# Performance work log

Measured on AMD Instinct MI355X. Metric: run time of the kernel, lower is better.

The kernel has to match this reference:

```python
import jax, jax.numpy as jnp
import numpy as np

B, T, D, H = 64, 512, 768, 96


def setup_inputs() -> dict:
    key = jax.random.key(0)
    kx, kq, kk, kv = jax.random.split(key, 4)
    x = jax.random.normal(kx, (B, T, D), dtype=jnp.float32)
    # Linear weights stored as [in, out]; scaled like torch default init
    s = 1.0 / np.sqrt(D)
    Wq = jax.random.normal(kq, (D, H), dtype=jnp.float32) * s
    Wk = jax.random.normal(kk, (D, H), dtype=jnp.float32) * s
    Wv = jax.random.normal(kv, (D, H), dtype=jnp.float32) * s
    return {"x": x, "Wq": Wq, "Wk": Wk, "Wv": Wv}


def reference(x, Wq, Wk, Wv):
    # q,k,v: [B,T,H]
    q = jnp.einsum('btd,dh->bth', x, Wq)
    k = jnp.einsum('btd,dh->bth', x, Wk)
    v = jnp.einsum('btd,dh->bth', x, Wv)
    scale = 1.0 / jnp.sqrt(jnp.array(q.shape[-1], dtype=x.dtype))
    # scores: [B,T,T]
    wei = jnp.einsum('bqh,bkh->bqk', q, k) * scale
    causal = jnp.tril(jnp.ones((T, T), dtype=bool))
    wei = jnp.where(causal, wei, jnp.array(-jnp.inf, dtype=wei.dtype))
    attn = jax.nn.softmax(wei, axis=-1)
    return jnp.einsum('bqk,bkh->bqh', attn, v)
```

## Files before the change

### kernel.cpp

```cpp
#include <hip/hip_runtime.h>
#include <hip/hip_bf16.h>
#include <math.h>

#define B_ 64
#define T_ 512
#define D_ 768
#define H_ 96
#define M_ (B_*T_)

typedef __attribute__((ext_vector_type(8))) short short8;
typedef __attribute__((ext_vector_type(4))) float f32x4;
typedef __attribute__((ext_vector_type(4))) unsigned uint4v;

__device__ __forceinline__ short f2bf(float f) {
  unsigned u = __float_as_uint(f);
  unsigned r = (u + 0x7FFFu + ((u >> 16) & 1u)) >> 16;
  return (short)r;
}

__device__ __forceinline__ unsigned cvtpk(float lo, float hi) {
  unsigned r;
  asm("v_cvt_pk_bf16_f32 %0, %1, %2" : "=v"(r) : "v"(lo), "v"(hi));
  return r;
}

__device__ __forceinline__ void gl16(const void* g, void* l) {
  __builtin_amdgcn_global_load_lds(
      (const __attribute__((address_space(1))) unsigned*)g,
      (__attribute__((address_space(3))) unsigned*)l, 16, 0, 0);
}

__global__ __launch_bounds__(256) void wt_kernel(
    const float* __restrict__ Wq, const float* __restrict__ Wk,
    const float* __restrict__ Wv, short* __restrict__ wt)
{
  int id = blockIdx.x * 256 + threadIdx.x;
  if (id >= 3*H_*D_) return;
  int n = id % 288;
  int k = id / 288;
  int mi = n / 96, cc = n % 96;
  const float* Wm = (mi == 0) ? Wq : ((mi == 1) ? Wk : Wv);
  wt[(size_t)n * D_ + k] = f2bf(Wm[(size_t)k * H_ + cc]);
}

#define BKP 32
#define ABYTES 8192
#define BBYTES 9216

__global__ __launch_bounds__(256) void qkv_mfma_kernel(
    const float* __restrict__ x, const short* __restrict__ wt,
    short* __restrict__ qb, short* __restrict__ kb, short* __restrict__ vb)
{
  __shared__ float As[2][64][32];
  __shared__ short Bs[2][144][32];

  const int t    = threadIdx.x;
  const int row0 = blockIdx.x * 64;
  const int cg   = blockIdx.y;
  const int lane = t & 63;
  const int w    = t >> 6;
  const int l15  = lane & 15;
  const int l4   = lane >> 4;

  auto stageA = [&](int buf, int k0) {
    #pragma unroll
    for (int i = 0; i < 2; ++i) {
      int inst = w * 2 + i;
      int row  = inst * 8 + (lane >> 3);
      int c16  = (lane & 7) ^ ((lane >> 3) & 7);
      const char* g = (const char*)(x + (size_t)(row0 + row) * D_ + k0) + c16 * 16;
      char* l = (char*)&As[buf][0][0] + inst * 1024 + lane * 16;
      gl16(g, l);
    }
  };
  auto stageB = [&](int buf, int k0) {
    #pragma unroll
    for (int i = 0; i < 3; ++i) {
      int inst = w + 4 * i;
      if (inst < 9) {
        int row = inst * 16 + (lane >> 2);
        int c16 = (lane & 3) ^ ((lane >> 2) & 3);
        const char* g = (const char*)(wt + (size_t)(cg * 144 + row) * D_ + k0) + c16 * 16;
        char* l = (char*)&Bs[buf][0][0] + inst * 1024 + lane * 16;
        gl16(g, l);
      }
    }
  };

  f32x4 acc[9];
  #pragma unroll
  for (int ci = 0; ci < 9; ++ci) acc[ci] = (f32x4){0.f, 0.f, 0.f, 0.f};

  stageA(0, 0);
  stageB(0, 0);
  __syncthreads();

  const int arow = w * 16 + l15;
  const char* Abase = (const char*)&As[0][0][0];
  const char* Bbase = (const char*)&Bs[0][0][0];

  for (int ks = 0; ks < 24; ++ks) {
    int buf = ks & 1;
    if (ks + 1 < 24) { stageA(buf ^ 1, (ks + 1) * BKP); stageB(buf ^ 1, (ks + 1) * BKP); }

    const char* ab = Abase + (size_t)buf * ABYTES + arow * 128;
    float4 a0 = *reinterpret_cast<const float4*>(ab + (((l4 * 2 + 0) ^ (arow & 7)) * 16));
    float4 a1 = *reinterpret_cast<const float4*>(ab + (((l4 * 2 + 1) ^ (arow & 7)) * 16));
    uint4v uv;
    uv[0] = cvtpk(a0.x, a0.y); uv[1] = cvtpk(a0.z, a0.w);
    uv[2] = cvtpk(a1.x, a1.y); uv[3] = cvtpk(a1.z, a1.w);
    short8 af = *reinterpret_cast<short8*>(&uv);

    #pragma unroll
    for (int ci = 0; ci < 9; ++ci) {
      int brow = ci * 16 + l15;
      short8 bf = *reinterpret_cast<const short8*>(
          Bbase + (size_t)buf * BBYTES + brow * 64 + ((l4 ^ (brow & 3)) * 16));
      acc[ci] = __builtin_amdgcn_mfma_f32_16x16x32_bf16(af, bf, acc[ci], 0, 0, 0);
    }
    __syncthreads();
  }

  const int rbase = row0 + w * 16 + l4 * 4;
  #pragma unroll
  for (int ci = 0; ci < 9; ++ci) {
    int ncol = cg * 144 + ci * 16;
    int mi   = ncol / 96;
    int cc   = ncol % 96 + l15;
    short* Om = (mi == 0) ? qb : ((mi == 1) ? kb : vb);
    #pragma unroll
    for (int reg = 0; reg < 4; ++reg)
      Om[(size_t)(rbase + reg) * H_ + cc] = f2bf(acc[ci][reg]);
  }
}

#define QB 32
#define KVB 32
#define KSTR 104
#define VSTR 40
#define PSTR 40

__global__ __launch_bounds__(128) void attn_mfma_kernel(
    const short* __restrict__ qb, const short* __restrict__ kb,
    const short* __restrict__ vb, float* __restrict__ out)
{
  __shared__ short ks[KVB][KSTR];
  __shared__ short vs[H_][VSTR];
  __shared__ short ps[2][16][PSTR];

  const int t    = threadIdx.x;
  const int lane = t & 63;
  const int w    = t >> 6;
  const int l15  = lane & 15;
  const int l4   = lane >> 4;
  const int qi   = 15 - blockIdx.x;
  const int b    = blockIdx.y;
  const int q0   = qi * QB;

  short8 qf[3];
  {
    const short* qbase = qb + ((size_t)(b * T_) + q0 + w * 16 + l15) * H_;
    #pragma unroll
    for (int f = 0; f < 3; ++f)
      qf[f] = *reinterpret_cast<const short8*>(qbase + f * 32 + l4 * 8);
  }

  f32x4 acc[6];
  #pragma unroll
  for (int c = 0; c < 6; ++c) acc[c] = (f32x4){0.f, 0.f, 0.f, 0.f};
  float m_r[4] = {-INFINITY, -INFINITY, -INFINITY, -INFINITY};
  float l_r[4] = {0.f, 0.f, 0.f, 0.f};
  const float scale = 0.10206207261596576f;

  const int jmax = q0 + QB;
  for (int j0 = 0; j0 < jmax; j0 += KVB) {
    __syncthreads();
    {
      int row = t >> 2, seg = t & 3;
      const short* src = kb + ((size_t)(b * T_) + j0 + row) * H_ + seg * 24;
      short* dst = &ks[row][seg * 24];
      *reinterpret_cast<short8*>(dst)      = *reinterpret_cast<const short8*>(src);
      *reinterpret_cast<short8*>(dst + 8)  = *reinterpret_cast<const short8*>(src + 8);
      *reinterpret_cast<short8*>(dst + 16) = *reinterpret_cast<const short8*>(src + 16);
    }
    {
      #pragma unroll
      for (int i = 0; i < 3; ++i) {
        int c = t + i * 128;
        int tok = c / 12;
        int m   = c % 12;
        int h0  = m * 8;
        short8 v = *reinterpret_cast<const short8*>(
            vb + (size_t)(b * T_ + j0 + tok) * H_ + h0);
        int tokS = tok ^ ((m & 3) << 3);
        #pragma unroll
        for (int j = 0; j < 8; ++j) vs[h0 + j][tokS] = v[j];
      }
    }
    __syncthreads();

    f32x4 sfr[2];
    sfr[0] = (f32x4){0.f,0.f,0.f,0.f};
    sfr[1] = (f32x4){0.f,0.f,0.f,0.f};
    #pragma unroll
    for (int ct = 0; ct < 2; ++ct)
      #pragma unroll
      for (int f = 0; f < 3; ++f) {
        short8 kf = *reinterpret_cast<const short8*>(&ks[ct * 16 + l15][f * 32 + l4 * 8]);
        sfr[ct] = __builtin_amdgcn_mfma_f32_16x16x32_bf16(qf[f], kf, sfr[ct], 0, 0, 0);
      }

    const int qrow = q0 + w * 16 + l4 * 4;
    float p0[4], p1[4], fsc[4];
    #pragma unroll
    for (int reg = 0; reg < 4; ++reg) {
      float s0 = sfr[0][reg] * scale;
      float s1 = sfr[1][reg] * scale;
      if (j0 + l15      > qrow + reg) s0 = -INFINITY;
      if (j0 + l15 + 16 > qrow + reg) s1 = -INFINITY;
      float tm = fmaxf(s0, s1);
      #pragma unroll
      for (int o = 1; o < 16; o <<= 1) tm = fmaxf(tm, __shfl_xor(tm, o));
      float Mnew = fmaxf(m_r[reg], tm);
      p0[reg] = __expf(s0 - Mnew);
      p1[reg] = __expf(s1 - Mnew);
      float psum = p0[reg] + p1[reg];
      #pragma unroll
      for (int o = 1; o < 16; o <<= 1) psum += __shfl_xor(psum, o);
      fsc[reg] = __expf(m_r[reg] - Mnew);
      m_r[reg] = Mnew;
      l_r[reg] = l_r[reg] * fsc[reg] + psum;
    }
    #pragma unroll
    for (int c = 0; c < 6; ++c)
      #pragma unroll
      for (int reg = 0; reg < 4; ++reg) acc[c][reg] *= fsc[reg];

    #pragma unroll
    for (int reg = 0; reg < 4; ++reg) {
      ps[w][l4 * 4 + reg][l15]      = f2bf(p0[reg]);
      ps[w][l4 * 4 + reg][l15 + 16] = f2bf(p1[reg]);
    }
    short8 pa = *reinterpret_cast<const short8*>(&ps[w][l15][l4 * 8]);

    #pragma unroll
    for (int c = 0; c < 6; ++c) {
      int h = c * 16 + l15;
      short8 vf = *reinterpret_cast<const short8*>(
          &vs[h][(l4 ^ ((h >> 3) & 3)) * 8]);
      acc[c] = __builtin_amdgcn_mfma_f32_16x16x32_bf16(pa, vf, acc[c], 0, 0, 0);
    }
  }

  float inv[4];
  #pragma unroll
  for (int reg = 0; reg < 4; ++reg) inv[reg] = 1.f / l_r[reg];
  #pragma unroll
  for (int c = 0; c < 6; ++c) {
    #pragma unroll
    for (int reg = 0; reg < 4; ++reg) {
      size_t row = (size_t)(b * T_) + q0 + w * 16 + l4 * 4 + reg;
      out[row * H_ + c * 16 + l15] = acc[c][reg] * inv[reg];
    }
  }
}

extern "C" void kernel_launch(void* const* d_in, const int* in_sizes, int n_in,
                              void* d_out, int out_size, void* d_ws, size_t ws_size,
                              hipStream_t stream) {
  const float* x  = (const float*)d_in[0];
  const float* Wq = (const float*)d_in[1];
  const float* Wk = (const float*)d_in[2];
  const float* Wv = (const float*)d_in[3];

  short* wt = (short*)d_ws;
  short* qb = (short*)((char*)d_ws + 524288);
  short* kb = qb + (size_t)M_ * H_;
  short* vb = kb + (size_t)M_ * H_;
  float* outp = (float*)d_out;

  hipLaunchKernelGGL(wt_kernel, dim3((3*H_*D_ + 255)/256), dim3(256), 0, stream,
                     Wq, Wk, Wv, wt);
  hipLaunchKernelGGL(qkv_mfma_kernel, dim3(M_/64, 2), dim3(256), 0, stream,
                     x, wt, qb, kb, vb);
  hipLaunchKernelGGL(attn_mfma_kernel, dim3(T_/QB, B_), dim3(128), 0, stream,
                     qb, kb, vb, outp);
}
```

Measured before the change: 79.35 us.

## Load full bf16 x tile once per block and cover all 288 QKV columns

The QKV projection kernel now converts a whole 64x768 fp32 x tile to bf16 in shared memory at the start, and each block computes all 288 output columns instead of splitting them across two blocks. This halves global reads of x, which were previously duplicated across the two column groups, and removes the per-step fp32-to-bf16 conversion from the main loop. Each wave now computes a 32x144 tile (two row fragments), so every loaded B fragment feeds two MFMAs. The cost is about 96KB of LDS for A plus 36KB for B, which lowers occupancy. The A tile is also loaded synchronously up front with no overlap with compute.

```diff
diff --git a/kernel.cpp b/kernel.cpp
--- a/kernel.cpp
+++ b/kernel.cpp
@@ -44,93 +44,100 @@
 }
 
 #define BKP 32
-#define ABYTES 8192
-#define BBYTES 9216
+#define BBYTES 18432
 
 __global__ __launch_bounds__(256) void qkv_mfma_kernel(
     const float* __restrict__ x, const short* __restrict__ wt,
     short* __restrict__ qb, short* __restrict__ kb, short* __restrict__ vb)
 {
-  __shared__ float As[2][64][32];
-  __shared__ short Bs[2][144][32];
+  __shared__ short Ab[64 * 768];
+  __shared__ short Bs[2][288][32];
 
   const int t    = threadIdx.x;
   const int row0 = blockIdx.x * 64;
-  const int cg   = blockIdx.y;
   const int lane = t & 63;
   const int w    = t >> 6;
+  const int wr   = w >> 1;
+  const int wc   = w & 1;
   const int l15  = lane & 15;
   const int l4   = lane >> 4;
 
-  auto stageA = [&](int buf, int k0) {
-    #pragma unroll
-    for (int i = 0; i < 2; ++i) {
-      int inst = w * 2 + i;
-      int row  = inst * 8 + (lane >> 3);
-      int c16  = (lane & 7) ^ ((lane >> 3) & 7);
-      const char* g = (const char*)(x + (size_t)(row0 + row) * D_ + k0) + c16 * 16;
-      char* l = (char*)&As[buf][0][0] + inst * 1024 + lane * 16;
-      gl16(g, l);
-    }
-  };
+  #pragma unroll
+  for (int i = 0; i < 24; ++i) {
+    int id  = t + i * 256;
+    int row = id / 96;
+    int c   = id % 96;
+    const float* src = x + (size_t)(row0 + row) * D_ + c * 8;
+    float4 f0 = *reinterpret_cast<const float4*>(src);
+    float4 f1 = *reinterpret_cast<const float4*>(src + 4);
+    uint4v uv;
+    uv[0] = cvtpk(f0.x, f0.y); uv[1] = cvtpk(f0.z, f0.w);
+    uv[2] = cvtpk(f1.x, f1.y); uv[3] = cvtpk(f1.z, f1.w);
+    *reinterpret_cast<short8*>(&Ab[row * 768 + ((c ^ (row & 7)) * 8)]) =
+        *reinterpret_cast<short8*>(&uv);
+  }
+
   auto stageB = [&](int buf, int k0) {
     #pragma unroll
-    for (int i = 0; i < 3; ++i) {
+    for (int i = 0; i < 5; ++i) {
       int inst = w + 4 * i;
-      if (inst < 9) {
+      if (inst < 18) {
         int row = inst * 16 + (lane >> 2);
         int c16 = (lane & 3) ^ ((lane >> 2) & 3);
-        const char* g = (const char*)(wt + (size_t)(cg * 144 + row) * D_ + k0) + c16 * 16;
+        const char* g = (const char*)(wt + (size_t)row * D_ + k0) + c16 * 16;
         char* l = (char*)&Bs[buf][0][0] + inst * 1024 + lane * 16;
         gl16(g, l);
       }
     }
   };
 
-  f32x4 acc[9];
-  #pragma unroll
-  for (int ci = 0; ci < 9; ++ci) acc[ci] = (f32x4){0.f, 0.f, 0.f, 0.f};
-
-  stageA(0, 0);
+  f32x4 acc[2][9];
+  #pragma unroll
+  for (int ri = 0; ri < 2; ++ri)
+    #pragma unroll
+    for (int ci = 0; ci < 9; ++ci) acc[ri][ci] = (f32x4){0.f, 0.f, 0.f, 0.f};
+
   stageB(0, 0);
   __syncthreads();
 
-  const int arow = w * 16 + l15;
-  const char* Abase = (const char*)&As[0][0][0];
   const char* Bbase = (const char*)&Bs[0][0][0];
 
   for (int ks = 0; ks < 24; ++ks) {
     int buf = ks & 1;
-    if (ks + 1 < 24) { stageA(buf ^ 1, (ks + 1) * BKP); stageB(buf ^ 1, (ks + 1) * BKP); }
-
-    const char* ab = Abase + (size_t)buf * ABYTES + arow * 128;
-    float4 a0 = *reinterpret_cast<const float4*>(ab + (((l4 * 2 + 0) ^ (arow & 7)) * 16));
-    float4 a1 = *reinterpret_cast<const float4*>(ab + (((l4 * 2 + 1) ^ (arow & 7)) * 16));
-    uint4v uv;
-    uv[0] = cvtpk(a0.x, a0.y); uv[1] = cvtpk(a0.z, a0.w);
-    uv[2] = cvtpk(a1.x, a1.y); uv[3] = cvtpk(a1.z, a1.w);
-    short8 af = *reinterpret_cast<short8*>(&uv);
-
+    if (ks + 1 < 24) stageB(buf ^ 1, (ks + 1) * BKP);
+
+    short8 af[2];
+    #pragma unroll
+    for (int ri = 0; ri < 2; ++ri) {
+      int row = wr * 32 + ri * 16 + l15;
+      int chunk = ks * 4 + l4;
+      af[ri] = *reinterpret_cast<const short8*>(
+          &Ab[row * 768 + ((chunk ^ (row & 7)) * 8)]);
+    }
     #pragma unroll
     for (int ci = 0; ci < 9; ++ci) {
-      int brow = ci * 16 + l15;
+      int brow = wc * 144 + ci * 16 + l15;
       short8 bf = *reinterpret_cast<const short8*>(
           Bbase + (size_t)buf * BBYTES + brow * 64 + ((l4 ^ (brow & 3)) * 16));
-      acc[ci] = __builtin_amdgcn_mfma_f32_16x16x32_bf16(af, bf, acc[ci], 0, 0, 0);
+      acc[0][ci] = __builtin_amdgcn_mfma_f32_16x16x32_bf16(af[0], bf, acc[0][ci], 0, 0, 0);
+      acc[1][ci] = __builtin_amdgcn_mfma_f32_16x16x32_bf16(af[1], bf, acc[1][ci], 0, 0, 0);
     }
     __syncthreads();
   }
 
-  const int rbase = row0 + w * 16 + l4 * 4;
   #pragma unroll
   for (int ci = 0; ci < 9; ++ci) {
-    int ncol = cg * 144 + ci * 16;
+    int ncol = wc * 144 + ci * 16;
     int mi   = ncol / 96;
     int cc   = ncol % 96 + l15;
     short* Om = (mi == 0) ? qb : ((mi == 1) ? kb : vb);
     #pragma unroll
-    for (int reg = 0; reg < 4; ++reg)
-      Om[(size_t)(rbase + reg) * H_ + cc] = f2bf(acc[ci][reg]);
+    for (int ri = 0; ri < 2; ++ri) {
+      int rbase = row0 + wr * 32 + ri * 16 + l4 * 4;
+      #pragma unroll
+      for (int reg = 0; reg < 4; ++reg)
+        Om[(size_t)(rbase + reg) * H_ + cc] = f2bf(acc[ri][ci][reg]);
+    }
   }
 }
 
@@ -281,7 +288,7 @@
 
   hipLaunchKernelGGL(wt_kernel, dim3((3*H_*D_ + 255)/256), dim3(256), 0, stream,
                      Wq, Wk, Wv, wt);
-  hipLaunchKernelGGL(qkv_mfma_kernel, dim3(M_/64, 2), dim3(256), 0, stream,
+  hipLaunchKernelGGL(qkv_mfma_kernel, dim3(M_/64), dim3(256), 0, stream,
                      x, wt, qb, kb, vb);
   hipLaunchKernelGGL(attn_mfma_kernel, dim3(T_/QB, B_), dim3(128), 0, stream,
                      qb, kb, vb, outp);
```

Result: slower. 97.13 us (+22.4%).
